# Optimization experiments

Hardware: AMD Instinct MI355X
Metric: run time of the kernel (lower is better)

## Reference

```python
import jax, jax.numpy as jnp
import numpy as np

NEAR, FAR, N_SAMPLES = 0.5, 10.0, 128
B, R, C = 8, 16384, 3


def setup_inputs() -> dict:
    key = jax.random.key(0)
    k1, k2 = jax.random.split(key)
    sigmas = jax.random.normal(k1, (B, R, N_SAMPLES, 1), dtype=jnp.float32)
    radiances = jax.random.uniform(k2, (B, R, N_SAMPLES, C), dtype=jnp.float32)
    z_vals = jnp.linspace(NEAR, FAR, N_SAMPLES, dtype=jnp.float32)  # [Z]
    return {"sigmas": sigmas, "radiances": radiances, "z_vals": z_vals}


def reference(sigmas, radiances, z_vals):
    # dists: [Z], last interval repeated (as in torch code)
    d = z_vals[1:] - z_vals[:-1]
    dists = jnp.concatenate([d, d[-1:]], axis=-1)
    # alpha = 1 - exp(-relu(sigma) * dist)  -> [B,R,Z,1]
    alpha = 1.0 - jnp.exp(-jax.nn.relu(sigmas) * dists[None, None, :, None])
    # shifted transmittance: prepend ones along Z, cumprod of (1-alpha+eps)
    alpha_shifted = jnp.concatenate(
        [jnp.ones_like(alpha[:, :, :1]), 1.0 - alpha + 1e-10], axis=-2
    )
    Ts = jnp.cumprod(alpha_shifted, axis=-2)
    weights = alpha * Ts[..., :-1, :]  # [B,R,Z,1]
    # rgb: einsum('brzs,brzs->brs') with s-broadcast => weighted sum over Z
    rgb = jnp.sum(weights * radiances, axis=-2)  # [B,R,C]
    depth_map = jnp.sum(weights * z_vals[None, None, :, None], axis=-2)  # [B,R,1]
    return rgb, depth_map, weights
```

## Files before the change

kernel.cpp:

```cpp
#include <hip/hip_runtime.h>
#include <cstddef>

#define NSAMP 128
#define WPB 4

typedef float f32x2 __attribute__((ext_vector_type(2)));

__global__ __launch_bounds__(256) void volrend_kernel(
    const float* __restrict__ sig,
    const float* __restrict__ rad,
    const float* __restrict__ zv,
    float* __restrict__ rgb,
    float* __restrict__ depth,
    float* __restrict__ wts,
    int n_rays)
{
    __shared__ float lds[WPB][384];

    const int lane = threadIdx.x & 63;
    const int wid  = threadIdx.x >> 6;
    int ray = blockIdx.x * WPB + wid;
    if (ray >= n_rays) ray = n_rays - 1;

    const int z0 = 2 * lane;

    const f32x2* rrow = (const f32x2*)(rad + (size_t)ray * 384);
    f32x2 r0 = __builtin_nontemporal_load(rrow + lane);
    f32x2 r1 = __builtin_nontemporal_load(rrow + 64 + lane);
    f32x2 r2 = __builtin_nontemporal_load(rrow + 128 + lane);
    f32x2* lrow = (f32x2*)lds[wid];
    lrow[lane]       = r0;
    lrow[64 + lane]  = r1;
    lrow[128 + lane] = r2;

    const f32x2 sv = __builtin_nontemporal_load(
        (const f32x2*)(sig + (size_t)ray * NSAMP) + lane);

    const f32x2 z01 = *((const f32x2*)zv + lane);
    const float z2  = zv[min(z0 + 2, 127)];
    const float d0  = z01.y - z01.x;
    const float d1  = (z0 + 1 < 127) ? (z2 - z01.y) : d0;

    const float e0 = __expf(-fmaxf(sv.x, 0.0f) * d0);
    const float e1 = __expf(-fmaxf(sv.y, 0.0f) * d1);
    const float a0 = 1.0f - e0;
    const float a1 = 1.0f - e1;
    const float f0 = e0 + 1e-10f;
    const float f1 = e1 + 1e-10f;

    float p = f0 * f1;
    #pragma unroll
    for (int d = 1; d < 64; d <<= 1) {
        float t = __shfl_up(p, d);
        if (lane >= d) p *= t;
    }
    float E = __shfl_up(p, 1);
    if (lane == 0) E = 1.0f;

    const float w0 = a0 * E;
    const float w1 = a1 * (E * f0);

    f32x2 wv; wv.x = w0; wv.y = w1;
    __builtin_nontemporal_store(wv, (f32x2*)(wts + (size_t)ray * NSAMP) + lane);

    __syncthreads();
    const float* lp = lds[wid] + 6 * lane;
    float s0 = w0 * lp[0] + w1 * lp[3];
    float s1 = w0 * lp[1] + w1 * lp[4];
    float s2 = w0 * lp[2] + w1 * lp[5];
    float s3 = w0 * z01.x + w1 * z01.y;

    s0 += __shfl_xor(s0, 32);
    s1 += __shfl_xor(s1, 32);
    s2 += __shfl_xor(s2, 32);
    s3 += __shfl_xor(s3, 32);
    float A = (lane & 32) ? s2 : s0;
    float B = (lane & 32) ? s3 : s1;
    A += __shfl_xor(A, 16);
    B += __shfl_xor(B, 16);
    float v = (lane & 16) ? B : A;
    v += __shfl_xor(v, 8);
    v += __shfl_xor(v, 4);
    v += __shfl_xor(v, 2);
    v += __shfl_xor(v, 1);

    if ((lane & 15) == 0) {
        const int c = lane >> 4;
        if (c < 3) rgb[(size_t)ray * 3 + c] = v;
        else       depth[ray] = v;
    }
}

extern "C" void kernel_launch(void* const* d_in, const int* in_sizes, int n_in,
                              void* d_out, int out_size, void* d_ws, size_t ws_size,
                              hipStream_t stream) {
    const float* sig = (const float*)d_in[0];
    const float* rad = (const float*)d_in[1];
    const float* zv  = (const float*)d_in[2];

    const int n_rays = in_sizes[0] / NSAMP;

    float* rgb   = (float*)d_out;
    float* depth = rgb + (size_t)n_rays * 3;
    float* wts   = depth + (size_t)n_rays;

    const int blocks = (n_rays + WPB - 1) / WPB;
    volrend_kernel<<<blocks, 64 * WPB, 0, stream>>>(
        sig, rad, zv, rgb, depth, wts, n_rays);
}
```

Baseline: 312.7 us.

## Process two rays per wavefront with four samples per lane and 128-bit loads

Each 64-lane wavefront now handles a pair of rays, with each half-wave covering one ray at four samples per lane. Radiance, sigma and weight traffic moves from 64-bit to 128-bit vector loads and stores. The prefix-product scan shrinks to 32 lanes and the reduction tree is shortened. The block-level barrier before reading LDS is dropped because each wave reads only what it wrote. The intent is fewer memory instructions and fewer waves per byte, at the cost of more registers per lane, and it assumes an even ray count.

```diff
diff --git a/kernel.cpp b/kernel.cpp
--- a/kernel.cpp
+++ b/kernel.cpp
@@ -4,7 +4,7 @@
 #define NSAMP 128
 #define WPB 4
 
-typedef float f32x2 __attribute__((ext_vector_type(2)));
+typedef float f32x4 __attribute__((ext_vector_type(4)));
 
 __global__ __launch_bounds__(256) void volrend_kernel(
     const float* __restrict__ sig,
@@ -13,81 +13,92 @@
     float* __restrict__ rgb,
     float* __restrict__ depth,
     float* __restrict__ wts,
-    int n_rays)
+    int n_pairs)
 {
-    __shared__ float lds[WPB][384];
+    __shared__ float lds[WPB][768];
 
     const int lane = threadIdx.x & 63;
     const int wid  = threadIdx.x >> 6;
-    int ray = blockIdx.x * WPB + wid;
-    if (ray >= n_rays) ray = n_rays - 1;
+    int rp = blockIdx.x * WPB + wid;
+    if (rp >= n_pairs) rp = n_pairs - 1;
 
-    const int z0 = 2 * lane;
+    const int sl  = lane & 31;
+    const int ray = 2 * rp + (lane >> 5);
 
-    const f32x2* rrow = (const f32x2*)(rad + (size_t)ray * 384);
-    f32x2 r0 = __builtin_nontemporal_load(rrow + lane);
-    f32x2 r1 = __builtin_nontemporal_load(rrow + 64 + lane);
-    f32x2 r2 = __builtin_nontemporal_load(rrow + 128 + lane);
-    f32x2* lrow = (f32x2*)lds[wid];
+    const f32x4* rbase = (const f32x4*)(rad + (size_t)rp * 768);
+    f32x4 r0 = __builtin_nontemporal_load(rbase + lane);
+    f32x4 r1 = __builtin_nontemporal_load(rbase + 64 + lane);
+    f32x4 r2 = __builtin_nontemporal_load(rbase + 128 + lane);
+    f32x4* lrow = (f32x4*)lds[wid];
     lrow[lane]       = r0;
     lrow[64 + lane]  = r1;
     lrow[128 + lane] = r2;
 
-    const f32x2 sv = __builtin_nontemporal_load(
-        (const f32x2*)(sig + (size_t)ray * NSAMP) + lane);
+    const f32x4 sv = __builtin_nontemporal_load(
+        (const f32x4*)(sig + (size_t)rp * 256) + lane);
 
-    const f32x2 z01 = *((const f32x2*)zv + lane);
-    const float z2  = zv[min(z0 + 2, 127)];
-    const float d0  = z01.y - z01.x;
-    const float d1  = (z0 + 1 < 127) ? (z2 - z01.y) : d0;
+    const f32x4 z4 = *((const f32x4*)zv + sl);
+    const float zn = zv[min(4 * sl + 4, 127)];
+    const float d0 = z4.y - z4.x;
+    const float d1 = z4.z - z4.y;
+    const float d2 = z4.w - z4.z;
+    const float d3 = (sl == 31) ? d2 : (zn - z4.w);
 
     const float e0 = __expf(-fmaxf(sv.x, 0.0f) * d0);
     const float e1 = __expf(-fmaxf(sv.y, 0.0f) * d1);
-    const float a0 = 1.0f - e0;
-    const float a1 = 1.0f - e1;
+    const float e2 = __expf(-fmaxf(sv.z, 0.0f) * d2);
+    const float e3 = __expf(-fmaxf(sv.w, 0.0f) * d3);
     const float f0 = e0 + 1e-10f;
     const float f1 = e1 + 1e-10f;
+    const float f2 = e2 + 1e-10f;
+    const float f3 = e3 + 1e-10f;
 
-    float p = f0 * f1;
+    const float F1 = f0;
+    const float F2 = f0 * f1;
+    const float F3 = F2 * f2;
+    float p = F3 * f3;
     #pragma unroll
-    for (int d = 1; d < 64; d <<= 1) {
+    for (int d = 1; d < 32; d <<= 1) {
         float t = __shfl_up(p, d);
-        if (lane >= d) p *= t;
+        if (sl >= d) p *= t;
     }
     float E = __shfl_up(p, 1);
-    if (lane == 0) E = 1.0f;
+    if (sl == 0) E = 1.0f;
 
-    const float w0 = a0 * E;
-    const float w1 = a1 * (E * f0);
+    const float w0 = (1.0f - e0) * E;
+    const float w1 = (1.0f - e1) * (E * F1);
+    const float w2 = (1.0f - e2) * (E * F2);
+    const float w3 = (1.0f - e3) * (E * F3);
 
-    f32x2 wv; wv.x = w0; wv.y = w1;
-    __builtin_nontemporal_store(wv, (f32x2*)(wts + (size_t)ray * NSAMP) + lane);
+    f32x4 wv; wv.x = w0; wv.y = w1; wv.z = w2; wv.w = w3;
+    __builtin_nontemporal_store(wv, (f32x4*)(wts + (size_t)rp * 256) + lane);
 
-    __syncthreads();
-    const float* lp = lds[wid] + 6 * lane;
-    float s0 = w0 * lp[0] + w1 * lp[3];
-    float s1 = w0 * lp[1] + w1 * lp[4];
-    float s2 = w0 * lp[2] + w1 * lp[5];
-    float s3 = w0 * z01.x + w1 * z01.y;
+    const f32x4* lp = (const f32x4*)(lds[wid] + (lane >> 5) * 384 + sl * 12);
+    const f32x4 ra = lp[0];
+    const f32x4 rb = lp[1];
+    const f32x4 rc = lp[2];
+    float s0 = w0 * ra.x + w1 * ra.w + w2 * rb.z + w3 * rc.y;
+    float s1 = w0 * ra.y + w1 * rb.x + w2 * rb.w + w3 * rc.z;
+    float s2 = w0 * ra.z + w1 * rb.y + w2 * rc.x + w3 * rc.w;
+    float s3 = w0 * z4.x + w1 * z4.y + w2 * z4.z + w3 * z4.w;
 
-    s0 += __shfl_xor(s0, 32);
-    s1 += __shfl_xor(s1, 32);
-    s2 += __shfl_xor(s2, 32);
-    s3 += __shfl_xor(s3, 32);
-    float A = (lane & 32) ? s2 : s0;
-    float B = (lane & 32) ? s3 : s1;
-    A += __shfl_xor(A, 16);
-    B += __shfl_xor(B, 16);
-    float v = (lane & 16) ? B : A;
-    v += __shfl_xor(v, 8);
-    v += __shfl_xor(v, 4);
-    v += __shfl_xor(v, 2);
-    v += __shfl_xor(v, 1);
+    s0 += __shfl_xor(s0, 16);
+    s1 += __shfl_xor(s1, 16);
+    s2 += __shfl_xor(s2, 16);
+    s3 += __shfl_xor(s3, 16);
+    float A = (sl & 16) ? s2 : s0;
+    float B = (sl & 16) ? s3 : s1;
+    A += __shfl_xor(A, 8);
+    B += __shfl_xor(B, 8);
+    float C = (sl & 8) ? B : A;
+    C += __shfl_xor(C, 4);
+    C += __shfl_xor(C, 2);
+    C += __shfl_xor(C, 1);
 
-    if ((lane & 15) == 0) {
-        const int c = lane >> 4;
-        if (c < 3) rgb[(size_t)ray * 3 + c] = v;
-        else       depth[ray] = v;
+    if ((sl & 7) == 0) {
+        const int c = sl >> 3;
+        if (c < 3) rgb[(size_t)ray * 3 + c] = C;
+        else       depth[ray] = C;
     }
 }
 
@@ -98,13 +109,14 @@
     const float* rad = (const float*)d_in[1];
     const float* zv  = (const float*)d_in[2];
 
-    const int n_rays = in_sizes[0] / NSAMP;
+    const int n_rays  = in_sizes[0] / NSAMP;
+    const int n_pairs = n_rays / 2;
 
     float* rgb   = (float*)d_out;
     float* depth = rgb + (size_t)n_rays * 3;
     float* wts   = depth + (size_t)n_rays;
 
-    const int blocks = (n_rays + WPB - 1) / WPB;
+    const int blocks = (n_pairs + WPB - 1) / WPB;
     volrend_kernel<<<blocks, 64 * WPB, 0, stream>>>(
-        sig, rad, zv, rgb, depth, wts, n_rays);
+        sig, rad, zv, rgb, depth, wts, n_pairs);
 }
```

Result: no change. 311.5 us (-0.4%).
